# Kernel optimization log

Hardware: AMD Instinct MI355X
Metric: run time of the kernel (lower is better)

The kernel has to match this reference:

```python
import jax, jax.numpy as jnp
from jax import lax
import numpy as np

B, T = 32, 64
E = 64        # embed_dim
U = 32        # num_measurements
D0, D1 = 300, 100
S = 9         # speaker_num
CELL = 64     # output_cell_dim
C = 6         # n_classes
EPS = 1e-12


def setup_inputs() -> dict:
    key = jax.random.key(0)
    ks = jax.random.split(key, 16)
    sc = 1.0 / np.sqrt(E)
    n = lambda i, shape, s=1.0: (jax.random.normal(ks[i], shape, jnp.float32) * s)
    return {
        "x0": n(0, (B, T, D0)),
        "x1": n(1, (B, T, D1)),
        "smask": jax.random.uniform(ks[2], (B, T, S), jnp.float32),
        "umask": jnp.ones((B, T), jnp.float32),
        "W_ih0": n(3, (4 * E, D0), sc), "W_hh0": n(4, (4 * E, E), sc),
        "b_ih0": n(5, (4 * E,), sc), "b_hh0": n(6, (4 * E,), sc),
        "W_ih1": n(7, (4 * E, D1), sc), "W_hh1": n(8, (4 * E, E), sc),
        "b_ih1": n(9, (4 * E,), sc), "b_hh1": n(10, (4 * E,), sc),
        "phase_table": jax.random.uniform(ks[11], (S, E), jnp.float32, -np.pi, np.pi),
        "meas_kernel": jax.random.uniform(ks[12], (U, E, 2), jnp.float32),
        "W1": n(13, (CELL, 2 * U), 0.1), "b1": jnp.zeros((CELL,), jnp.float32),
        "W2": n(14, (C, CELL), 0.1), "b2": jnp.zeros((C,), jnp.float32),
    }


def _lstm_tanh(x, um, Wih, Whh, bih, bhh):
    # torch.nn.LSTMCell (gate order i,f,g,o) + extra tanh applied to h each step;
    # the tanh-ed h is carried as the recurrent state (dropout = identity in eval).
    b, t, _ = x.shape
    e = Whh.shape[1]

    def step(carry, inp):
        h, c = carry
        xt, ut = inp
        g = (xt * ut[:, None]) @ Wih.T + bih + h @ Whh.T + bhh
        i, f, gg, o = jnp.split(g, 4, axis=-1)
        c = jax.nn.sigmoid(f) * c + jax.nn.sigmoid(i) * jnp.tanh(gg)
        h = jnp.tanh(jax.nn.sigmoid(o) * jnp.tanh(c))
        return (h, c), h

    h0 = jnp.zeros((b, e), x.dtype)
    _, hs = lax.scan(step, (h0, h0), (jnp.swapaxes(x, 0, 1), um.T))
    return jnp.swapaxes(hs, 0, 1)  # (B,T,E)


def _measure(amp, phase, kernel):
    # pure state v = cos(phase)*amp + i sin(phase)*amp; rho = |v><v|
    r = jnp.cos(phase) * amp
    im = jnp.sin(phase) * amp
    rho_r = jnp.einsum('bti,btj->btij', r, r) + jnp.einsum('bti,btj->btij', im, im)
    rho_i = jnp.einsum('bti,btj->btij', im, r) - jnp.einsum('bti,btj->btij', r, im)
    u = kernel.shape[0]
    norm = jnp.clip(jnp.linalg.norm(kernel.reshape(u, -1), axis=-1), EPS)
    kn = kernel / norm[:, None, None]
    kr, ki = kn[..., 0], kn[..., 1]
    Pr = jnp.einsum('ui,uj->uij', kr, kr) + jnp.einsum('ui,uj->uij', ki, ki)
    Pi = jnp.einsum('ui,uj->uij', ki, kr) - jnp.einsum('ui,uj->uij', kr, ki)
    return jnp.einsum('btij,uij->btu', rho_r, Pr) - jnp.einsum('btij,uij->btu', rho_i, Pi)


def reference(x0, x1, smask, umask, W_ih0, W_hh0, b_ih0, b_hh0,
              W_ih1, W_hh1, b_ih1, b_hh1, phase_table, meas_kernel,
              W1, b1, W2, b2):
    h0 = _lstm_tanh(x0, umask, W_ih0, W_hh0, b_ih0, b_hh0)
    h1 = _lstm_tanh(x1, umask, W_ih1, W_hh1, b_ih1, b_hh1)
    norm = lambda h: h / jnp.clip(jnp.linalg.norm(h, axis=-1, keepdims=True), EPS)
    phase = phase_table[jnp.argmax(smask, axis=-1)]  # (B,T,E); table shared by both modalities
    m = jnp.concatenate([_measure(norm(h0), phase, meas_kernel),
                         _measure(norm(h1), phase, meas_kernel)], axis=-1)
    hid = jax.nn.relu(m @ W1.T + b1)
    pred = jnp.tanh(hid @ W2.T + b2)
    return jax.nn.log_softmax(pred, axis=2)
```

## Files before the change

### kernel.cpp

```cpp
#include <hip/hip_runtime.h>

typedef unsigned short ushort_t;
typedef unsigned int uint_t;

__device__ __forceinline__ float bf2f(ushort_t v) {
  union { uint_t u; float f; } x; x.u = ((uint_t)v) << 16; return x.f;
}
__device__ __forceinline__ float lo16(uint_t u) {
  union { uint_t u; float f; } x; x.u = u << 16; return x.f;
}
__device__ __forceinline__ float hi16(uint_t u) {
  union { uint_t u; float f; } x; x.u = u & 0xffff0000u; return x.f;
}
__device__ __forceinline__ ushort_t f2bf(float f) {
  union { float f; uint_t u; } x; x.f = f;
  uint_t u = x.u;
  uint_t r = (u + 0x7fffu + ((u >> 16) & 1u)) >> 16;
  return (ushort_t)r;
}
__device__ __forceinline__ bool is_bf16(const void* um) {
  return *(const uint_t*)um == 0x3F803F80u;
}
__device__ __forceinline__ float ld_dual(const void* p, int i, bool isb) {
  return isb ? bf2f(((const ushort_t*)p)[i]) : ((const float*)p)[i];
}
__device__ __forceinline__ float fsig(float x) { return 1.f / (1.f + __expf(-x)); }
__device__ __forceinline__ float ftanh(float x) { return 2.f / (1.f + __expf(-2.f * x)) - 1.f; }

__device__ __forceinline__ float dpp_add_xor1(float v) {
  const int r = __builtin_amdgcn_update_dpp(0, __float_as_int(v), 0xB1, 0xF, 0xF, true);
  return v + __int_as_float(r);
}
__device__ __forceinline__ float dpp_add_xor2(float v) {
  const int r = __builtin_amdgcn_update_dpp(0, __float_as_int(v), 0x4E, 0xF, 0xF, true);
  return v + __int_as_float(r);
}

template <int D, bool ISB>
__device__ __forceinline__ void proj_body(
    const void* __restrict__ x, const void* __restrict__ um,
    const void* __restrict__ Wih, const void* __restrict__ bih,
    const void* __restrict__ bhh, float* __restrict__ xw, float* xs)
{
  const int tid = threadIdx.x;
  const int r0 = blockIdx.x * 8;
  for (int i = tid; i < 8 * D; i += 256) {
    const int r = i / D;
    xs[i] = ld_dual(x, r0 * D + i, ISB) * ld_dual(um, r0 + r, ISB);
  }
  __syncthreads();
  float acc[8];
#pragma unroll
  for (int r = 0; r < 8; ++r) acc[r] = 0.f;
#pragma unroll 5
  for (int k = 0; k < D; k += 4) {
    float w0, w1, w2, w3;
    if (ISB) {
      const ushort_t* wr = (const ushort_t*)Wih + tid * D;
      const uint2 wu = *(const uint2*)(wr + k);
      w0 = lo16(wu.x); w1 = hi16(wu.x); w2 = lo16(wu.y); w3 = hi16(wu.y);
    } else {
      const float* wr = (const float*)Wih + tid * D;
      const float4 wv = *(const float4*)(wr + k);
      w0 = wv.x; w1 = wv.y; w2 = wv.z; w3 = wv.w;
    }
#pragma unroll
    for (int r = 0; r < 8; ++r) {
      const float4 xv = *(const float4*)(xs + r * D + k);
      acc[r] = fmaf(xv.x, w0, acc[r]);
      acc[r] = fmaf(xv.y, w1, acc[r]);
      acc[r] = fmaf(xv.z, w2, acc[r]);
      acc[r] = fmaf(xv.w, w3, acc[r]);
    }
  }
  const float bias = ld_dual(bih, tid, ISB) + ld_dual(bhh, tid, ISB);
  const int pos = ((tid & 63) << 2) | (tid >> 6);
#pragma unroll
  for (int r = 0; r < 8; ++r)
    xw[(r0 + r) * 256 + pos] = acc[r] + bias;
}

__global__ __launch_bounds__(256) void proj_both(
    const void* __restrict__ x0, const void* __restrict__ x1,
    const void* __restrict__ um,
    const void* __restrict__ Wih0, const void* __restrict__ bih0,
    const void* __restrict__ bhh0,
    const void* __restrict__ Wih1, const void* __restrict__ bih1,
    const void* __restrict__ bhh1,
    float* __restrict__ xw0, float* __restrict__ xw1)
{
  __shared__ __align__(16) float xs[8 * 300];
  const bool isb = is_bf16(um);
  if (blockIdx.y == 0) {
    if (isb) proj_body<300, true>(x0, um, Wih0, bih0, bhh0, xw0, xs);
    else     proj_body<300, false>(x0, um, Wih0, bih0, bhh0, xw0, xs);
  } else {
    if (isb) proj_body<100, true>(x1, um, Wih1, bih1, bhh1, xw1, xs);
    else     proj_body<100, false>(x1, um, Wih1, bih1, bhh1, xw1, xs);
  }
}

__global__ __launch_bounds__(256, 1) void lstm_k(
    const float* __restrict__ xw0, const float* __restrict__ xw1,
    const void* __restrict__ Whh0, const void* __restrict__ Whh1,
    const void* __restrict__ um,
    float* __restrict__ h0r, float* __restrict__ h1r)
{
  __shared__ __align__(16) float xws[64 * 256];
  __shared__ __align__(16) float hist[65 * 64];

  const int bid = blockIdx.x;
  const int l = bid >> 5;
  const int b = bid & 31;
  const float* xw = (l ? xw1 : xw0) + b * 64 * 256;
  const void* Whh = (l ? Whh1 : Whh0);
  float* hr = (l ? h1r : h0r) + b * 64 * 64;
  const int tid = threadIdx.x;
  const int e = tid >> 2;
  const int q = tid & 3;
  const int k0 = q << 4;
  const bool isb = is_bf16(um);

  for (int i = tid; i < 4096; i += 256)
    *(float4*)(xws + i * 4) = *(const float4*)(xw + i * 4);
  if (tid < 64) hist[tid] = 0.f;

  float w[4][16];
  if (isb) {
#pragma unroll
    for (int t = 0; t < 4; ++t) {
      const ushort_t* wr = (const ushort_t*)Whh + (t * 64 + e) * 64 + k0;
#pragma unroll
      for (int j = 0; j < 16; j += 8) {
        const uint4 v = *(const uint4*)(wr + j);
        w[t][j + 0] = lo16(v.x); w[t][j + 1] = hi16(v.x);
        w[t][j + 2] = lo16(v.y); w[t][j + 3] = hi16(v.y);
        w[t][j + 4] = lo16(v.z); w[t][j + 5] = hi16(v.z);
        w[t][j + 6] = lo16(v.w); w[t][j + 7] = hi16(v.w);
      }
    }
  } else {
#pragma unroll
    for (int t = 0; t < 4; ++t) {
      const float* wr = (const float*)Whh + (t * 64 + e) * 64 + k0;
#pragma unroll
      for (int j = 0; j < 16; j += 4) {
        const float4 v = *(const float4*)(wr + j);
        w[t][j + 0] = v.x; w[t][j + 1] = v.y;
        w[t][j + 2] = v.z; w[t][j + 3] = v.w;
      }
    }
  }
  __syncthreads();

  float c = 0.f;
  for (int s = 0; s < 64; ++s) {
    const float gin = xws[s * 256 + tid];
    const float* hp = hist + s * 64 + k0;
    float p0 = 0.f, p1 = 0.f, p2 = 0.f, p3 = 0.f;
#pragma unroll
    for (int j = 0; j < 16; j += 4) {
      const float4 hv = *(const float4*)(hp + j);
      p0 = fmaf(w[0][j + 0], hv.x, p0); p0 = fmaf(w[0][j + 1], hv.y, p0);
      p0 = fmaf(w[0][j + 2], hv.z, p0); p0 = fmaf(w[0][j + 3], hv.w, p0);
      p1 = fmaf(w[1][j + 0], hv.x, p1); p1 = fmaf(w[1][j + 1], hv.y, p1);
      p1 = fmaf(w[1][j + 2], hv.z, p1); p1 = fmaf(w[1][j + 3], hv.w, p1);
      p2 = fmaf(w[2][j + 0], hv.x, p2); p2 = fmaf(w[2][j + 1], hv.y, p2);
      p2 = fmaf(w[2][j + 2], hv.z, p2); p2 = fmaf(w[2][j + 3], hv.w, p2);
      p3 = fmaf(w[3][j + 0], hv.x, p3); p3 = fmaf(w[3][j + 1], hv.y, p3);
      p3 = fmaf(w[3][j + 2], hv.z, p3); p3 = fmaf(w[3][j + 3], hv.w, p3);
    }
    if (q == 0) p0 += gin;
    else if (q == 1) p1 += gin;
    else if (q == 2) p2 += gin;
    else p3 += gin;
    p0 = dpp_add_xor1(p0); p0 = dpp_add_xor2(p0);
    p1 = dpp_add_xor1(p1); p1 = dpp_add_xor2(p1);
    p2 = dpp_add_xor1(p2); p2 = dpp_add_xor2(p2);
    p3 = dpp_add_xor1(p3); p3 = dpp_add_xor2(p3);
    const float yi = fsig(p0);
    const float yf = fsig(p1);
    const float yg = ftanh(p2);
    const float yo = fsig(p3);
    c = fmaf(yf, c, yi * yg);
    const float h = ftanh(yo * ftanh(c));
    if (q == 0) hist[(s + 1) * 64 + e] = h;
    __syncthreads();
  }
  for (int i = tid; i < 1024; i += 256)
    *(float4*)(hr + i * 4) = *(const float4*)(hist + 64 + i * 4);
}

__global__ __launch_bounds__(256) void head_k(
    const float* __restrict__ h0r, const float* __restrict__ h1r,
    const void* __restrict__ smask, const void* __restrict__ um,
    const void* __restrict__ ptab, const void* __restrict__ mker,
    const void* __restrict__ W1, const void* __restrict__ b1,
    const void* __restrict__ W2, const void* __restrict__ b2,
    void* __restrict__ out)
{
  __shared__ float2 knT[64][32];
  __shared__ float w1T[64][64];
  __shared__ float w2T[64][8];
  __shared__ float b1s[64];
  __shared__ float b2s[8];
  __shared__ float rim[4][4][64];
  __shared__ float msh[4][64];
  __shared__ float hidsh[4][64];
  __shared__ float psh[4][8];

  const int tid = threadIdx.x;
  const bool isb = is_bf16(um);
  {
    const int u = tid >> 3, sub = tid & 7;
    float vr[8], vi[8];
    float ssq = 0.f;
#pragma unroll
    for (int qq = 0; qq < 8; ++qq) {
      const int e = sub * 8 + qq;
      if (isb) {
        const uint_t kk = ((const uint_t*)mker)[u * 64 + e];
        vr[qq] = lo16(kk); vi[qq] = hi16(kk);
      } else {
        const float2 kk = ((const float2*)mker)[u * 64 + e];
        vr[qq] = kk.x; vi[qq] = kk.y;
      }
      ssq = fmaf(vr[qq], vr[qq], ssq);
      ssq = fmaf(vi[qq], vi[qq], ssq);
    }
    ssq += __shfl_xor(ssq, 1);
    ssq += __shfl_xor(ssq, 2);
    ssq += __shfl_xor(ssq, 4);
    const float rn = 1.f / fmaxf(sqrtf(ssq), 1e-12f);
#pragma unroll
    for (int qq = 0; qq < 8; ++qq) {
      const int e = sub * 8 + qq;
      knT[e][u] = make_float2(vr[qq] * rn, vi[qq] * rn);
    }
  }
  for (int i = tid; i < 4096; i += 256) {
    const int j = i >> 6, ll = i & 63;
    w1T[ll][j] = ld_dual(W1, i, isb);
  }
  if (tid < 64) b1s[tid] = ld_dual(b1, tid, isb);
  for (int i = tid; i < 384; i += 256) {
    const int cc = i >> 6, j = i & 63;
    w2T[j][cc] = ld_dual(W2, i, isb);
  }
  if (tid < 6) b2s[tid] = ld_dual(b2, tid, isb);
  __syncthreads();

  const int wv = tid >> 6, lane = tid & 63;
  const int item = blockIdx.x * 4 + wv;
  const float h0raw = h0r[item * 64 + lane];
  const float h1raw = h1r[item * 64 + lane];
  float ss0 = h0raw * h0raw, ss1 = h1raw * h1raw;
#pragma unroll
  for (int m = 1; m < 64; m <<= 1) {
    ss0 += __shfl_xor(ss0, m);
    ss1 += __shfl_xor(ss1, m);
  }
  const float h0 = h0raw / fmaxf(sqrtf(ss0), 1e-12f);
  const float h1 = h1raw / fmaxf(sqrtf(ss1), 1e-12f);

  int idx = 0;
  if (lane == 0) {
    float best = -1e30f;
#pragma unroll
    for (int si = 0; si < 9; ++si) {
      const float v = ld_dual(smask, item * 9 + si, isb);
      if (v > best) { best = v; idx = si; }
    }
  }
  idx = __shfl(idx, 0, 64);
  const float ph = ld_dual(ptab, idx * 64 + lane, isb);
  float sr, cr;
  __sincosf(ph, &sr, &cr);
  rim[wv][0][lane] = cr * h0;
  rim[wv][1][lane] = sr * h0;
  rim[wv][2][lane] = cr * h1;
  rim[wv][3][lane] = sr * h1;
  __syncthreads();
  {
    const int u = lane & 31;
    const float* ra = rim[wv][(lane >= 32) ? 2 : 0];
    const float* ia = rim[wv][(lane >= 32) ? 3 : 1];
    float ar = 0.f, ai = 0.f;
#pragma unroll 8
    for (int e = 0; e < 64; ++e) {
      const float2 k = knT[e][u];
      const float rr = ra[e], ii = ia[e];
      ar = fmaf(rr, k.x, ar);
      ar = fmaf(-ii, k.y, ar);
      ai = fmaf(rr, k.y, ai);
      ai = fmaf(ii, k.x, ai);
    }
    msh[wv][lane] = fmaf(ar, ar, ai * ai);
  }
  __syncthreads();
  {
    float acc = b1s[lane];
#pragma unroll 8
    for (int L = 0; L < 64; ++L)
      acc = fmaf(msh[wv][L], w1T[L][lane], acc);
    hidsh[wv][lane] = fmaxf(acc, 0.f);
  }
  __syncthreads();
  if (lane < 6) {
    float a2 = b2s[lane];
#pragma unroll 8
    for (int j = 0; j < 64; ++j)
      a2 = fmaf(hidsh[wv][j], w2T[j][lane], a2);
    psh[wv][lane] = ftanh(a2);
  }
  __syncthreads();
  if (lane < 6) {
    const float p = psh[wv][lane];
    float mx = psh[wv][0];
#pragma unroll
    for (int cc = 1; cc < 6; ++cc) mx = fmaxf(mx, psh[wv][cc]);
    float sum = 0.f;
#pragma unroll
    for (int cc = 0; cc < 6; ++cc) sum += __expf(psh[wv][cc] - mx);
    const float res = p - mx - __logf(sum);
    if (isb) ((ushort_t*)out)[item * 6 + lane] = f2bf(res);
    else     ((float*)out)[item * 6 + lane] = res;
  }
}

extern "C" void kernel_launch(void* const* d_in, const int* in_sizes, int n_in,
                              void* d_out, int out_size, void* d_ws, size_t ws_size,
                              hipStream_t stream)
{
  (void)in_sizes; (void)n_in; (void)out_size; (void)ws_size;
  const void* x0    = d_in[0];
  const void* x1    = d_in[1];
  const void* smask = d_in[2];
  const void* um    = d_in[3];
  const void* Wih0  = d_in[4];
  const void* Whh0  = d_in[5];
  const void* bih0  = d_in[6];
  const void* bhh0  = d_in[7];
  const void* Wih1  = d_in[8];
  const void* Whh1  = d_in[9];
  const void* bih1  = d_in[10];
  const void* bhh1  = d_in[11];
  const void* ptab  = d_in[12];
  const void* mker  = d_in[13];
  const void* W1    = d_in[14];
  const void* b1    = d_in[15];
  const void* W2    = d_in[16];
  const void* b2    = d_in[17];

  float* xw0 = (float*)d_ws;
  float* xw1 = xw0 + 2048 * 256;
  float* h0r = xw1 + 2048 * 256;
  float* h1r = h0r + 2048 * 64;

  hipLaunchKernelGGL(proj_both, dim3(256, 2), dim3(256), 0, stream,
                     x0, x1, um, Wih0, bih0, bhh0, Wih1, bih1, bhh1,
                     xw0, xw1);
  hipLaunchKernelGGL(lstm_k, dim3(64), dim3(256), 0, stream,
                     xw0, xw1, Whh0, Whh1, um, h0r, h1r);
  hipLaunchKernelGGL(head_k, dim3(512), dim3(256), 0, stream,
                     h0r, h1r, smask, um, ptab, mker, W1, b1, W2, b2,
                     d_out);
}
```

Before: 165.4 us.

## Fuse LSTM recurrence and measurement head into one kernel per batch

Merges the LSTM and head kernels into one kernel. Each block of 512 threads runs both modality LSTMs for one batch element and keeps the hidden states in shared memory. The head then reads those states from shared memory instead of global memory, with each wave handling 8 timesteps in turn. To fit in shared memory, the input projections are staged in two halves, with a reload and barrier at step 32. This removes a kernel launch and the global round-trip of the hidden states. In exchange, the head runs on only 32 blocks, and each per-step barrier now spans 8 waves.

```diff
diff --git a/kernel.cpp b/kernel.cpp
--- a/kernel.cpp
+++ b/kernel.cpp
@@ -100,30 +100,32 @@
   }
 }
 
-__global__ __launch_bounds__(256, 1) void lstm_k(
+__global__ __launch_bounds__(512, 1) void fused_k(
     const float* __restrict__ xw0, const float* __restrict__ xw1,
     const void* __restrict__ Whh0, const void* __restrict__ Whh1,
     const void* __restrict__ um,
-    float* __restrict__ h0r, float* __restrict__ h1r)
+    const void* __restrict__ smask, const void* __restrict__ ptab,
+    const void* __restrict__ mker,
+    const void* __restrict__ W1, const void* __restrict__ b1,
+    const void* __restrict__ W2, const void* __restrict__ b2,
+    void* __restrict__ out)
 {
-  __shared__ __align__(16) float xws[64 * 256];
-  __shared__ __align__(16) float hist[65 * 64];
-
-  const int bid = blockIdx.x;
-  const int l = bid >> 5;
-  const int b = bid & 31;
+  __shared__ __align__(16) float hist[2][65 * 64];
+  __shared__ __align__(16) char scratch[65536];
+
+  const int b = blockIdx.x;
+  const int tid = threadIdx.x;
+  const int l = tid >> 8;
+  const int tid2 = tid & 255;
+  const int e = tid2 >> 2;
+  const int q = tid2 & 3;
+  const int k0 = q << 4;
+  const bool isb = is_bf16(um);
+
   const float* xw = (l ? xw1 : xw0) + b * 64 * 256;
   const void* Whh = (l ? Whh1 : Whh0);
-  float* hr = (l ? h1r : h0r) + b * 64 * 64;
-  const int tid = threadIdx.x;
-  const int e = tid >> 2;
-  const int q = tid & 3;
-  const int k0 = q << 4;
-  const bool isb = is_bf16(um);
-
-  for (int i = tid; i < 4096; i += 256)
-    *(float4*)(xws + i * 4) = *(const float4*)(xw + i * 4);
-  if (tid < 64) hist[tid] = 0.f;
+  float* xws = (float*)scratch + l * 32 * 256;
+  float* hl = hist[l];
 
   float w[4][16];
   if (isb) {
@@ -151,12 +153,21 @@
       }
     }
   }
+  if (tid2 < 64) hl[tid2] = 0.f;
+  for (int i = tid2; i < 2048; i += 256)
+    *(float4*)(xws + i * 4) = *(const float4*)(xw + i * 4);
   __syncthreads();
 
   float c = 0.f;
+#pragma unroll 1
   for (int s = 0; s < 64; ++s) {
-    const float gin = xws[s * 256 + tid];
-    const float* hp = hist + s * 64 + k0;
+    if (s == 32) {
+      for (int i = tid2; i < 2048; i += 256)
+        *(float4*)(xws + i * 4) = *(const float4*)(xw + 8192 + i * 4);
+      __syncthreads();
+    }
+    const float gin = xws[(s & 31) * 256 + tid2];
+    const float* hp = hl + s * 64 + k0;
     float p0 = 0.f, p1 = 0.f, p2 = 0.f, p3 = 0.f;
 #pragma unroll
     for (int j = 0; j < 16; j += 4) {
@@ -184,45 +195,32 @@
     const float yo = fsig(p3);
     c = fmaf(yf, c, yi * yg);
     const float h = ftanh(yo * ftanh(c));
-    if (q == 0) hist[(s + 1) * 64 + e] = h;
+    if (q == 0) hl[(s + 1) * 64 + e] = h;
     __syncthreads();
   }
-  for (int i = tid; i < 1024; i += 256)
-    *(float4*)(hr + i * 4) = *(const float4*)(hist + 64 + i * 4);
-}
-
-__global__ __launch_bounds__(256) void head_k(
-    const float* __restrict__ h0r, const float* __restrict__ h1r,
-    const void* __restrict__ smask, const void* __restrict__ um,
-    const void* __restrict__ ptab, const void* __restrict__ mker,
-    const void* __restrict__ W1, const void* __restrict__ b1,
-    const void* __restrict__ W2, const void* __restrict__ b2,
-    void* __restrict__ out)
-{
-  __shared__ float2 knT[64][32];
-  __shared__ float w1T[64][64];
-  __shared__ float w2T[64][8];
-  __shared__ float b1s[64];
-  __shared__ float b2s[8];
-  __shared__ float rim[4][4][64];
-  __shared__ float msh[4][64];
-  __shared__ float hidsh[4][64];
-  __shared__ float psh[4][8];
-
-  const int tid = threadIdx.x;
-  const bool isb = is_bf16(um);
-  {
+
+  float2 (*knT)[32] = (float2(*)[32])scratch;
+  float (*w1T)[64]  = (float(*)[64])(scratch + 16384);
+  float (*w2T)[8]   = (float(*)[8])(scratch + 32768);
+  float* b1s        = (float*)(scratch + 34816);
+  float* b2s        = (float*)(scratch + 35072);
+  float (*rim)[4][64] = (float(*)[4][64])(scratch + 35328);
+  float (*msh)[64]  = (float(*)[64])(scratch + 43520);
+  float (*hidsh)[64] = (float(*)[64])(scratch + 45568);
+  float (*psh)[8]   = (float(*)[8])(scratch + 47616);
+
+  if (tid < 256) {
     const int u = tid >> 3, sub = tid & 7;
     float vr[8], vi[8];
     float ssq = 0.f;
 #pragma unroll
     for (int qq = 0; qq < 8; ++qq) {
-      const int e = sub * 8 + qq;
+      const int ee = sub * 8 + qq;
       if (isb) {
-        const uint_t kk = ((const uint_t*)mker)[u * 64 + e];
+        const uint_t kk = ((const uint_t*)mker)[u * 64 + ee];
         vr[qq] = lo16(kk); vi[qq] = hi16(kk);
       } else {
-        const float2 kk = ((const float2*)mker)[u * 64 + e];
+        const float2 kk = ((const float2*)mker)[u * 64 + ee];
         vr[qq] = kk.x; vi[qq] = kk.y;
       }
       ssq = fmaf(vr[qq], vr[qq], ssq);
@@ -234,16 +232,16 @@
     const float rn = 1.f / fmaxf(sqrtf(ssq), 1e-12f);
 #pragma unroll
     for (int qq = 0; qq < 8; ++qq) {
-      const int e = sub * 8 + qq;
-      knT[e][u] = make_float2(vr[qq] * rn, vi[qq] * rn);
-    }
-  }
-  for (int i = tid; i < 4096; i += 256) {
+      const int ee = sub * 8 + qq;
+      knT[ee][u] = make_float2(vr[qq] * rn, vi[qq] * rn);
+    }
+  }
+  for (int i = tid; i < 4096; i += 512) {
     const int j = i >> 6, ll = i & 63;
     w1T[ll][j] = ld_dual(W1, i, isb);
   }
   if (tid < 64) b1s[tid] = ld_dual(b1, tid, isb);
-  for (int i = tid; i < 384; i += 256) {
+  for (int i = tid; i < 384; i += 512) {
     const int cc = i >> 6, j = i & 63;
     w2T[j][cc] = ld_dual(W2, i, isb);
   }
@@ -251,80 +249,80 @@
   __syncthreads();
 
   const int wv = tid >> 6, lane = tid & 63;
-  const int item = blockIdx.x * 4 + wv;
-  const float h0raw = h0r[item * 64 + lane];
-  const float h1raw = h1r[item * 64 + lane];
-  float ss0 = h0raw * h0raw, ss1 = h1raw * h1raw;
-#pragma unroll
-  for (int m = 1; m < 64; m <<= 1) {
-    ss0 += __shfl_xor(ss0, m);
-    ss1 += __shfl_xor(ss1, m);
-  }
-  const float h0 = h0raw / fmaxf(sqrtf(ss0), 1e-12f);
-  const float h1 = h1raw / fmaxf(sqrtf(ss1), 1e-12f);
-
-  int idx = 0;
-  if (lane == 0) {
-    float best = -1e30f;
-#pragma unroll
-    for (int si = 0; si < 9; ++si) {
-      const float v = ld_dual(smask, item * 9 + si, isb);
-      if (v > best) { best = v; idx = si; }
-    }
-  }
-  idx = __shfl(idx, 0, 64);
-  const float ph = ld_dual(ptab, idx * 64 + lane, isb);
-  float sr, cr;
-  __sincosf(ph, &sr, &cr);
-  rim[wv][0][lane] = cr * h0;
-  rim[wv][1][lane] = sr * h0;
-  rim[wv][2][lane] = cr * h1;
-  rim[wv][3][lane] = sr * h1;
-  __syncthreads();
-  {
-    const int u = lane & 31;
-    const float* ra = rim[wv][(lane >= 32) ? 2 : 0];
-    const float* ia = rim[wv][(lane >= 32) ? 3 : 1];
-    float ar = 0.f, ai = 0.f;
+#pragma unroll 1
+  for (int it = 0; it < 8; ++it) {
+    const int titem = wv * 8 + it;
+    const int item = b * 64 + titem;
+    const float h0raw = hist[0][(titem + 1) * 64 + lane];
+    const float h1raw = hist[1][(titem + 1) * 64 + lane];
+    float ss0 = h0raw * h0raw, ss1 = h1raw * h1raw;
+#pragma unroll
+    for (int m = 1; m < 64; m <<= 1) {
+      ss0 += __shfl_xor(ss0, m);
+      ss1 += __shfl_xor(ss1, m);
+    }
+    const float h0 = h0raw / fmaxf(sqrtf(ss0), 1e-12f);
+    const float h1 = h1raw / fmaxf(sqrtf(ss1), 1e-12f);
+
+    int idx = 0;
+    if (lane == 0) {
+      float best = -1e30f;
+#pragma unroll
+      for (int si = 0; si < 9; ++si) {
+        const float v = ld_dual(smask, item * 9 + si, isb);
+        if (v > best) { best = v; idx = si; }
+      }
+    }
+    idx = __shfl(idx, 0, 64);
+    const float ph = ld_dual(ptab, idx * 64 + lane, isb);
+    float sr, cr;
+    __sincosf(ph, &sr, &cr);
+    rim[wv][0][lane] = cr * h0;
+    rim[wv][1][lane] = sr * h0;
+    rim[wv][2][lane] = cr * h1;
+    rim[wv][3][lane] = sr * h1;
+    {
+      const int u = lane & 31;
+      const float* ra = rim[wv][(lane >= 32) ? 2 : 0];
+      const float* ia = rim[wv][(lane >= 32) ? 3 : 1];
+      float ar = 0.f, ai = 0.f;
 #pragma unroll 8
-    for (int e = 0; e < 64; ++e) {
-      const float2 k = knT[e][u];
-      const float rr = ra[e], ii = ia[e];
-      ar = fmaf(rr, k.x, ar);
-      ar = fmaf(-ii, k.y, ar);
-      ai = fmaf(rr, k.y, ai);
-      ai = fmaf(ii, k.x, ai);
-    }
-    msh[wv][lane] = fmaf(ar, ar, ai * ai);
-  }
-  __syncthreads();
-  {
-    float acc = b1s[lane];
+      for (int ee = 0; ee < 64; ++ee) {
+        const float2 k = knT[ee][u];
+        const float rr = ra[ee], ii = ia[ee];
+        ar = fmaf(rr, k.x, ar);
+        ar = fmaf(-ii, k.y, ar);
+        ai = fmaf(rr, k.y, ai);
+        ai = fmaf(ii, k.x, ai);
+      }
+      msh[wv][lane] = fmaf(ar, ar, ai * ai);
+    }
+    {
+      float acc = b1s[lane];
 #pragma unroll 8
-    for (int L = 0; L < 64; ++L)
-      acc = fmaf(msh[wv][L], w1T[L][lane], acc);
-    hidsh[wv][lane] = fmaxf(acc, 0.f);
-  }
-  __syncthreads();
-  if (lane < 6) {
-    float a2 = b2s[lane];
+      for (int L = 0; L < 64; ++L)
+        acc = fmaf(msh[wv][L], w1T[L][lane], acc);
+      hidsh[wv][lane] = fmaxf(acc, 0.f);
+    }
+    if (lane < 6) {
+      float a2 = b2s[lane];
 #pragma unroll 8
-    for (int j = 0; j < 64; ++j)
-      a2 = fmaf(hidsh[wv][j], w2T[j][lane], a2);
-    psh[wv][lane] = ftanh(a2);
-  }
-  __syncthreads();
-  if (lane < 6) {
-    const float p = psh[wv][lane];
-    float mx = psh[wv][0];
-#pragma unroll
-    for (int cc = 1; cc < 6; ++cc) mx = fmaxf(mx, psh[wv][cc]);
-    float sum = 0.f;
-#pragma unroll
-    for (int cc = 0; cc < 6; ++cc) sum += __expf(psh[wv][cc] - mx);
-    const float res = p - mx - __logf(sum);
-    if (isb) ((ushort_t*)out)[item * 6 + lane] = f2bf(res);
-    else     ((float*)out)[item * 6 + lane] = res;
+      for (int j = 0; j < 64; ++j)
+        a2 = fmaf(hidsh[wv][j], w2T[j][lane], a2);
+      psh[wv][lane] = ftanh(a2);
+    }
+    if (lane < 6) {
+      const float p = psh[wv][lane];
+      float mx = psh[wv][0];
+#pragma unroll
+      for (int cc = 1; cc < 6; ++cc) mx = fmaxf(mx, psh[wv][cc]);
+      float sum = 0.f;
+#pragma unroll
+      for (int cc = 0; cc < 6; ++cc) sum += __expf(psh[wv][cc] - mx);
+      const float res = p - mx - __logf(sum);
+      if (isb) ((ushort_t*)out)[item * 6 + lane] = f2bf(res);
+      else     ((float*)out)[item * 6 + lane] = res;
+    }
   }
 }
 
@@ -354,15 +352,11 @@
 
   float* xw0 = (float*)d_ws;
   float* xw1 = xw0 + 2048 * 256;
-  float* h0r = xw1 + 2048 * 256;
-  float* h1r = h0r + 2048 * 64;
 
   hipLaunchKernelGGL(proj_both, dim3(256, 2), dim3(256), 0, stream,
                      x0, x1, um, Wih0, bih0, bhh0, Wih1, bih1, bhh1,
                      xw0, xw1);
-  hipLaunchKernelGGL(lstm_k, dim3(64), dim3(256), 0, stream,
-                     xw0, xw1, Whh0, Whh1, um, h0r, h1r);
-  hipLaunchKernelGGL(head_k, dim3(512), dim3(256), 0, stream,
-                     h0r, h1r, smask, um, ptab, mker, W1, b1, W2, b2,
-                     d_out);
-}
+  hipLaunchKernelGGL(fused_k, dim3(32), dim3(512), 0, stream,
+                     xw0, xw1, Whh0, Whh1, um,
+                     smask, ptab, mker, W1, b1, W2, b2, d_out);
+}
```

Result: slower. 204.7 us (+23.7%).
